# Kernel optimization log

Measured on AMD Instinct MI355X. Metric: run time of the kernel, lower is better.

Reference implementation:

```python
import jax, jax.numpy as jnp
import numpy as np

BINS = 32
NUM_ACTION = 12


def _conv(x, w, b, stride, pad):
    y = jax.lax.conv_general_dilated(x, w, (stride, stride), [(pad, pad), (pad, pad)],
                                     dimension_numbers=('NCHW', 'OIHW', 'NCHW'))
    return y + b[None, :, None, None]


def _maxpool3s2(x):
    return jax.lax.reduce_window(x, -jnp.inf, jax.lax.max, (1, 1, 3, 3), (1, 1, 2, 2), 'VALID')


def _area_resize(x, oh, ow):
    b, c, h, w = x.shape  # exact area interp when h%oh==0, w%ow==0
    return x.reshape(b, c, oh, h // oh, ow, w // ow).mean(axis=(3, 5))


def _sobel_mag(gray):
    # kornia.filters.Sobel: normalized sobel kernels (abs-sum=1), replicate pad, sqrt(gx^2+gy^2+eps)
    kx = jnp.array([[-1., 0., 1.], [-2., 0., 2.], [-1., 0., 1.]], jnp.float32) / 8.0
    k = jnp.stack([kx, kx.T])[:, None]  # [2,1,3,3]
    p = jnp.pad(gray, ((0, 0), (0, 0), (1, 1), (1, 1)), mode='edge')
    g = jax.lax.conv_general_dilated(p, k, (1, 1), 'VALID',
                                     dimension_numbers=('NCHW', 'OIHW', 'NCHW'))
    return jnp.sqrt(jnp.sum(g * g, axis=1, keepdims=True) + 1e-6)


def _hist_feature(img):
    # Fused replacement for FeatureExtractor's python triple-loop of torch.histc calls.
    # img: [B,1,H,W] with values in [0,1]. Scale 0: whole-image hist; scale 1: the 4
    # quadrants of the full-res image; third bins-slot stays zero (loop only runs 2 scales).
    b, _, h, w = img.shape
    idx = jnp.clip((img[:, 0] * BINS).astype(jnp.int32), 0, BINS - 1)  # [B,H,W]
    hist = lambda i: jnp.zeros((BINS,), jnp.float32).at[i.ravel()].add(1.0)
    h0 = jax.vmap(hist)(idx) / (h * w)                                  # [B,BINS]
    h2, w2 = h // 2, w // 2
    blocks = idx.reshape(b, 2, h2, 2, w2).transpose(0, 1, 3, 2, 4).reshape(b * 4, h2 * w2)
    h1 = jax.vmap(hist)(blocks).reshape(b, 2, 2, BINS) / (h2 * w2)      # [B,2,2,BINS]
    out0 = jnp.broadcast_to(h0[:, :, None, None], (b, BINS, 4, 4))
    out1 = jnp.repeat(jnp.repeat(h1.transpose(0, 3, 1, 2), 2, axis=2), 2, axis=3)
    out2 = jnp.zeros_like(out0)
    return jnp.concatenate([out0, out1, out2], axis=1)                  # [B,3*BINS,4,4]


def _l2norm(x):
    return x / (jnp.linalg.norm(x, axis=1, keepdims=True) + 1e-7)


def _forward(image, w1, b1, w2, b2, w3, b3, w4, b4, w5, b5, fc1_w, fc1_b, fc2_w, fc2_b):
    b = image.shape[0]
    rgb = jnp.stack([image[:, 0], 0.5 * (image[:, 1] + image[:, 2]), image[:, 3]], axis=1)
    # AlexNet conv backbone on area-resized 112x112 -> [B,256,2,2]
    x = _area_resize(rgb, 112, 112)
    x = _maxpool3s2(jax.nn.relu(_conv(x, w1, b1, 4, 2)))
    x = _maxpool3s2(jax.nn.relu(_conv(x, w2, b2, 1, 2)))
    x = jax.nn.relu(_conv(x, w3, b3, 1, 1))
    x = jax.nn.relu(_conv(x, w4, b4, 1, 1))
    x = _maxpool3s2(jax.nn.relu(_conv(x, w5, b5, 1, 1)))
    f_sem = x.reshape(b, -1)                                            # [B,1024]
    gray = (0.299 * rgb[:, 0] + 0.587 * rgb[:, 1] + 0.114 * rgb[:, 2])[:, None]
    f_inten = _hist_feature(gray).reshape(b, -1)                        # [B,1536]
    f_grad = _hist_feature(_sobel_mag(gray)).reshape(b, -1)             # [B,1536]
    f_cat = jnp.concatenate([_l2norm(f_sem), _l2norm(f_inten), _l2norm(f_grad)], axis=1)
    h = jax.nn.relu(f_cat)                                              # Dropout = identity (eval)
    h = jax.nn.relu(h @ fc1_w.T + fc1_b)
    return h @ fc2_w.T + fc2_b                                          # [B,NUM_ACTION]


def setup_inputs() -> dict:
    key = jax.random.key(0)
    ks = jax.random.split(key, 8)
    B = 64
    image = jax.random.uniform(ks[0], (B, 4, 448, 448), jnp.float32)
    w = lambda k, shape, s=0.02: jax.random.normal(k, shape, jnp.float32) * s
    return {
        'image': image,
        'w1': w(ks[1], (64, 3, 11, 11)), 'b1': jnp.zeros((64,), jnp.float32),
        'w2': w(ks[2], (192, 64, 5, 5)), 'b2': jnp.zeros((192,), jnp.float32),
        'w3': w(ks[3], (384, 192, 3, 3)), 'b3': jnp.zeros((384,), jnp.float32),
        'w4': w(ks[4], (256, 384, 3, 3)), 'b4': jnp.zeros((256,), jnp.float32),
        'w5': w(ks[5], (256, 256, 3, 3)), 'b5': jnp.zeros((256,), jnp.float32),
        'fc1_w': w(ks[6], (256, 4096), 0.01), 'fc1_b': jnp.zeros((256,), jnp.float32),
        'fc2_w': w(ks[7], (NUM_ACTION, 256), 0.05), 'fc2_b': jnp.zeros((NUM_ACTION,), jnp.float32),
    }


def reference(image, w1, b1, w2, b2, w3, b3, w4, b4, w5, b5, fc1_w, fc1_b, fc2_w, fc2_b):
    return _forward(image, w1, b1, w2, b2, w3, b3, w4, b4, w5, b5, fc1_w, fc1_b, fc2_w, fc2_b)
```

## Files before the change

kernel.cpp:

```cpp
#include <hip/hip_runtime.h>
#include <math.h>

typedef __attribute__((ext_vector_type(8))) short short8;
typedef __attribute__((ext_vector_type(8))) unsigned short u16x8;
typedef __attribute__((ext_vector_type(4))) float f32x4;
typedef unsigned short ushort_t;

constexpr size_t OFF_HINT = 0;
constexpr size_t OFF_HGRD = OFF_HINT + (size_t)64*160;
constexpr size_t OFF_F    = OFF_HGRD + (size_t)64*160;
constexpr size_t OFF_H1   = OFF_F    + (size_t)64*4096;
constexpr size_t OFF_P5   = OFF_H1   + (size_t)64*256;
constexpr size_t OFF_WHI  = OFF_P5   + (size_t)64*1024;
constexpr size_t W1_OFF = 0;         constexpr int K1T = 363,  K1R = 384;
constexpr size_t W2_OFF = 24576;     constexpr int K2T = 1600, K2R = 1664;
constexpr size_t W3_OFF = 344064;    constexpr int K3T = 1728, K3R = 1792;
constexpr size_t W4_OFF = 1032192;   constexpr int K4T = 3456, K4R = 3456;
constexpr size_t W5_OFF = 1916928;   constexpr int K5T = 2304, K5R = 2304;
constexpr size_t WP_U16 = 2506752;
constexpr size_t OFF_WLO  = OFF_WHI + WP_U16/2;
constexpr size_t OFF_RA   = OFF_WLO + WP_U16/2;
constexpr size_t SZ_RA    = (size_t)2583552/2;
constexpr size_t A4P_U16  = 786432;
constexpr size_t OFF_RB   = OFF_RA + SZ_RA;
constexpr size_t SZ_RB    = (size_t)2985984/2;
constexpr size_t WS_FLOATS = OFF_RB + SZ_RB;

__device__ __forceinline__ void bf16split(float v, unsigned short& hi, unsigned short& lo) {
  union { float f; unsigned u; } a; a.f = v;
  unsigned uh = (a.u + 0x7FFFu + ((a.u >> 16) & 1u)) >> 16;
  hi = (unsigned short)uh;
  union { unsigned u; float f; } b; b.u = uh << 16;
  float rem = v - b.f;
  union { float f; unsigned u; } c; c.f = rem;
  lo = (unsigned short)((c.u + 0x7FFFu + ((c.u >> 16) & 1u)) >> 16);
}
__device__ __forceinline__ ushort_t f2bf(float f) {
  union { float f; unsigned u; } a; a.f = f;
  return (ushort_t)((a.u + 0x7FFFu + ((a.u >> 16) & 1u)) >> 16);
}
__device__ __forceinline__ float bf2f(ushort_t u) {
  union { unsigned u; float f; } a; a.u = ((unsigned)u) << 16; return a.f;
}

__global__ __launch_bounds__(256) void k_wsplit_all(const float* __restrict__ w1,
                                                    const float* __restrict__ w2,
                                                    const float* __restrict__ w3,
                                                    const float* __restrict__ w4,
                                                    const float* __restrict__ w5,
                                                    ushort_t* __restrict__ whi,
                                                    ushort_t* __restrict__ wlo) {
  const size_t idx = (size_t)blockIdx.x * 256 + threadIdx.x;
  if (idx >= WP_U16) return;
  const float* w; int kt, kr; size_t base;
  if (idx < W2_OFF)                { w = w1; kt = K1T; kr = K1R; base = W1_OFF; }
  else if (idx < W3_OFF)           { w = w2; kt = K2T; kr = K2R; base = W2_OFF; }
  else if (idx < W4_OFF)           { w = w3; kt = K3T; kr = K3R; base = W3_OFF; }
  else if (idx < W5_OFF)           { w = w4; kt = K4T; kr = K4R; base = W4_OFF; }
  else                             { w = w5; kt = K5T; kr = K5R; base = W5_OFF; }
  const size_t rel = idx - base;
  const int m = (int)(rel / kr), k = (int)(rel - (size_t)m * kr);
  const float v = (k < kt) ? w[(size_t)m * kt + k] : 0.f;
  unsigned short h, l;
  bf16split(v, h, l);
  whi[idx] = h; wlo[idx] = l;
}

__global__ __launch_bounds__(256) void k_preproc(const float* __restrict__ img,
                                                 float* __restrict__ hint,
                                                 float* __restrict__ hgrd,
                                                 ushort_t* __restrict__ x0) {
  const int b = blockIdx.x, s = blockIdx.y;
  const int r0 = s * 8;
  __shared__ float gs[10][448];
  __shared__ unsigned char lh[128 * 260];
  __shared__ float part[8 * 112 * 3];
  const int tid = threadIdx.x;
  for (int i = tid; i < (128 * 260) / 4; i += 256) ((unsigned*)lh)[i] = 0u;
  const float* ib = img + (size_t)b * 4 * 200704;
  for (int i = tid; i < 10 * 112; i += 256) {
    const int rr = i / 112, cc = i % 112, c4 = cc * 4;
    int r = r0 + rr - 1; r = r < 0 ? 0 : (r > 447 ? 447 : r);
    const size_t o = (size_t)r * 448 + c4;
    const float4 vr = *(const float4*)&ib[o];
    const float4 g1 = *(const float4*)&ib[200704 + o];
    const float4 g2 = *(const float4*)&ib[2 * 200704 + o];
    const float4 vb = *(const float4*)&ib[3 * 200704 + o];
    float4 g;
    g.x = 0.299f * vr.x + 0.587f * (0.5f * (g1.x + g2.x)) + 0.114f * vb.x;
    g.y = 0.299f * vr.y + 0.587f * (0.5f * (g1.y + g2.y)) + 0.114f * vb.y;
    g.z = 0.299f * vr.z + 0.587f * (0.5f * (g1.z + g2.z)) + 0.114f * vb.z;
    g.w = 0.299f * vr.w + 0.587f * (0.5f * (g1.w + g2.w)) + 0.114f * vb.w;
    *(float4*)&gs[rr][c4] = g;
    if (rr >= 1 && rr <= 8) {
      const float sr = vr.x + vr.y + vr.z + vr.w;
      const float sg = 0.5f * (g1.x + g2.x) + 0.5f * (g1.y + g2.y)
                     + 0.5f * (g1.z + g2.z) + 0.5f * (g1.w + g2.w);
      const float sb = vb.x + vb.y + vb.z + vb.w;
      float* pp = &part[((rr - 1) * 112 + cc) * 3];
      pp[0] = sr; pp[1] = sg; pp[2] = sb;
    }
  }
  __syncthreads();
  for (int i = tid; i < 8 * 112; i += 256) {
    const int dr = i / 112, c4 = (i % 112) * 4;
    const unsigned colbit = (c4 >= 224) ? 1u : 0u;
    const int cl = c4 > 0 ? c4 - 1 : 0;
    const int cr = c4 < 444 ? c4 + 4 : 447;
    const float4 m0 = *(const float4*)&gs[dr][c4];
    const float4 m1 = *(const float4*)&gs[dr + 1][c4];
    const float4 m2 = *(const float4*)&gs[dr + 2][c4];
    const float r0v[6] = {gs[dr][cl],     m0.x, m0.y, m0.z, m0.w, gs[dr][cr]};
    const float r1v[6] = {gs[dr + 1][cl], m1.x, m1.y, m1.z, m1.w, gs[dr + 1][cr]};
    const float r2v[6] = {gs[dr + 2][cl], m2.x, m2.y, m2.z, m2.w, gs[dr + 2][cr]};
    #pragma unroll
    for (int j = 0; j < 4; ++j) {
      const float g = r1v[j + 1];
      int bin = (int)(g * 32.f); bin = bin > 31 ? 31 : (bin < 0 ? 0 : bin);
      lh[(colbit * 32u + (unsigned)bin) * 260u + (unsigned)tid]++;
      const float gx = (-r0v[j] + r0v[j + 2] - 2.f * r1v[j] + 2.f * r1v[j + 2]
                        - r2v[j] + r2v[j + 2]) * 0.125f;
      const float gy = (-r0v[j] - 2.f * r0v[j + 1] - r0v[j + 2]
                        + r2v[j] + 2.f * r2v[j + 1] + r2v[j + 2]) * 0.125f;
      const float mag = sqrtf(gx * gx + gy * gy + 1e-6f);
      int sb = (int)(mag * 32.f); sb = sb > 31 ? 31 : (sb < 0 ? 0 : sb);
      lh[(64u + colbit * 32u + (unsigned)sb) * 260u + (unsigned)tid]++;
    }
  }
  __syncthreads();
  {
    const unsigned rowbit = (s >= 28) ? 1u : 0u;
    const int key = tid >> 1, half = tid & 1;
    const unsigned* row = (const unsigned*)&lh[(unsigned)key * 260u];
    unsigned sum = 0;
    #pragma unroll
    for (int d = 0; d < 32; ++d) {
      const unsigned v = row[half * 32 + d];
      sum += (v & 0xFFu) + ((v >> 8) & 0xFFu) + ((v >> 16) & 0xFFu) + (v >> 24);
    }
    sum += __shfl_down(sum, 1, 64);
    if (half == 0) {
      const int type = key >> 6;
      const int rest = key & 63;
      const int colbit2 = rest >> 5, bin = rest & 31;
      float* dst = (type ? hgrd : hint) + (size_t)b * 160 + 32 + (rowbit * 2 + colbit2) * 32 + bin;
      atomicAdd(dst, (float)sum);
    }
  }
  for (int i = tid; i < 672; i += 256) {
    const int cc = i % 112;
    const int t  = i / 112;
    const int or2 = t & 1, ch = t >> 1;
    float sum = 0.f;
    #pragma unroll
    for (int rw = 0; rw < 4; ++rw)
      sum += part[((or2 * 4 + rw) * 112 + cc) * 3 + ch];
    x0[(((size_t)b * 3 + ch) * 116 + 2 + 2 * s + or2) * 116 + 2 + cc] = f2bf(sum * (1.f / 16.f));
  }
}

template<int CIN, int HP, int WP, int KH, int KW, int STRIDE, int OH, int OW,
         int OHP, int OWP, int OPAD, int M, int MT>
__global__ __launch_bounds__(512) void k_conv_mfma(const ushort_t* __restrict__ in,
                                                   const ushort_t* __restrict__ whi_,
                                                   const ushort_t* __restrict__ wlo_,
                                                   const float* __restrict__ bias,
                                                   ushort_t* __restrict__ out) {
  constexpr int K_TOT  = CIN * KH * KW;
  constexpr int K_ROUND = ((K_TOT + 127) / 128) * 128;
  constexpr int GSTEPS = K_ROUND / 128;
  constexpr int KHW = KH * KW;
  constexpr int NPB = OH * OW;
  constexpr int WROWS = MT / 16;
  constexpr int TGRP  = 4 / WROWS;
  constexpr int TFRAG = 4 / TGRP;
  __shared__ ushort_t Bs[2][64 * 64];
  __shared__ ushort_t ftab[K_ROUND];
  const int tid = threadIdx.x;
  const int lane = tid & 63, wv = tid >> 6;
  const int g = wv >> 2, wg = wv & 3;
  const int sub = tid & 255;
  const int n0 = blockIdx.x * 64, m0 = blockIdx.y * MT;
  for (int k = tid; k < K_ROUND; k += 512) {
    const int c = k / KHW, kr = k - c * KHW;
    const int ky = kr / KW, kx = kr - (kr / KW) * KW;
    ftab[k] = (k < K_TOT) ? (ushort_t)(2 * ((c * HP + ky) * WP + kx)) : (ushort_t)0;
  }
  const int col = sub & 63, kc2 = sub >> 6;
  const int nb = n0 + col;
  const int bB = nb / NPB, rB = nb % NPB;
  const int oyB = rB / OW, oxB = rB % OW;
  const char* baseB = (const char*)(in + (size_t)bB * CIN * HP * WP)
                      + 2 * (oyB * STRIDE * WP + oxB * STRIDE);
  const int wm = wg % WROWS, tg = wg / WROWS;
  const int mrow = m0 + wm * 16 + (lane & 15);
  const ushort_t* wh = whi_ + (size_t)mrow * K_ROUND;
  const ushort_t* wl = wlo_ + (size_t)mrow * K_ROUND;
  const int kA = (lane >> 4) * 8;
  f32x4 acc[TFRAG] = {};
  __syncthreads();
  const int kb0 = g * GSTEPS * 64;
  for (int step = 0; step < GSTEPS; ++step) {
    const int kb = kb0 + step * 64;
    const u16x8 f0 = *(const u16x8*)&ftab[kb + kc2 * 16];
    const u16x8 f1 = *(const u16x8*)&ftab[kb + kc2 * 16 + 8];
    u16x8 b0, b1;
    #pragma unroll
    for (int j = 0; j < 8; ++j) b0[j] = *(const ushort_t*)(baseB + f0[j]);
    #pragma unroll
    for (int j = 0; j < 8; ++j) b1[j] = *(const ushort_t*)(baseB + f1[j]);
    const int c0 = kc2 * 2, c1 = c0 + 1;
    *(u16x8*)&Bs[g][col * 64 + ((c0 ^ (col & 7)) * 8)] = b0;
    *(u16x8*)&Bs[g][col * 64 + ((c1 ^ (col & 7)) * 8)] = b1;
    __syncthreads();
    #pragma unroll
    for (int s = 0; s < 2; ++s) {
      const int kk = kb + s * 32 + kA;
      const short8 a_h = *(const short8*)&wh[kk];
      const short8 a_l = *(const short8*)&wl[kk];
      const int cA = s * 4 + (lane >> 4);
      #pragma unroll
      for (int tt = 0; tt < TFRAG; ++tt) {
        const int t = tg * TFRAG + tt;
        const int coln = t * 16 + (lane & 15);
        const short8 b_v = *(const short8*)&Bs[g][coln * 64 + ((cA ^ (coln & 7)) * 8)];
        acc[tt] = __builtin_amdgcn_mfma_f32_16x16x32_bf16(a_h, b_v, acc[tt], 0, 0, 0);
        acc[tt] = __builtin_amdgcn_mfma_f32_16x16x32_bf16(a_l, b_v, acc[tt], 0, 0, 0);
      }
    }
    __syncthreads();
  }
  float* scratch = (float*)&Bs[0][0];
  if (g == 1) {
    #pragma unroll
    for (int tt = 0; tt < TFRAG; ++tt) {
      const int t = tg * TFRAG + tt;
      #pragma unroll
      for (int q = 0; q < 4; ++q)
        scratch[(wm * 16 + (lane >> 4) * 4 + q) * 64 + t * 16 + (lane & 15)] = acc[tt][q];
    }
  }
  __syncthreads();
  if (g == 0) {
    #pragma unroll
    for (int q = 0; q < 4; ++q) {
      const int m = m0 + wm * 16 + (lane >> 4) * 4 + q;
      const float bi = bias[m];
      #pragma unroll
      for (int tt = 0; tt < TFRAG; ++tt) {
        const int t = tg * TFRAG + tt;
        const int n = n0 + t * 16 + (lane & 15);
        const float v = acc[tt][q]
                      + scratch[(wm * 16 + (lane >> 4) * 4 + q) * 64 + t * 16 + (lane & 15)]
                      + bi;
        const int b = n / NPB, r = n % NPB;
        const int oy = r / OW, ox = r - (r / OW) * OW;
        out[(((size_t)b * M + m) * OHP + OPAD + oy) * OWP + OPAD + ox] = f2bf(fmaxf(v, 0.f));
      }
    }
  }
}

template<int C, int HI, int HO, int HOP, int PAD, bool OUTF32>
__global__ __launch_bounds__(256) void k_pool(const ushort_t* __restrict__ in,
                                              void* __restrict__ out) {
  const int idx = blockIdx.x * 256 + threadIdx.x;
  constexpr int TOT = 64 * C * HOP * HOP;
  if (idx >= TOT) return;
  const int x = idx % HOP;
  const int y = (idx / HOP) % HOP;
  const int c = (idx / (HOP * HOP)) % C;
  const int b = idx / (HOP * HOP * C);
  ushort_t v = 0;
  const int oy = y - PAD, ox = x - PAD;
  if (oy >= 0 && oy < HO && ox >= 0 && ox < HO) {
    const ushort_t* ib = in + (size_t)(b * C + c) * HI * HI + (size_t)(oy * 2) * HI + ox * 2;
    #pragma unroll
    for (int i = 0; i < 3; ++i)
      #pragma unroll
      for (int j = 0; j < 3; ++j) {
        const ushort_t u = ib[i * HI + j];
        v = u > v ? u : v;
      }
  }
  if constexpr (OUTF32) ((float*)out)[idx] = bf2f(v);
  else                  ((ushort_t*)out)[idx] = v;
}

__global__ __launch_bounds__(256) void k_feat(const float* __restrict__ p5,
                                              const float* __restrict__ hint,
                                              const float* __restrict__ hgrad,
                                              float* __restrict__ f) {
  const int b = blockIdx.x, tid = threadIdx.x;
  __shared__ float tmp4[4];
  __shared__ float vals[160];
  const float* ps = p5 + (size_t)b * 1024;
  float* fb = f + (size_t)b * 4096;
  float mv[4]; float ss = 0.f;
  #pragma unroll
  for (int i = 0; i < 4; ++i) { mv[i] = ps[tid + i * 256]; ss += mv[i] * mv[i]; }
  #pragma unroll
  for (int o = 32; o > 0; o >>= 1) ss += __shfl_down(ss, o, 64);
  if ((tid & 63) == 0) tmp4[tid >> 6] = ss;
  __syncthreads();
  const float inv = 1.f / (sqrtf(tmp4[0] + tmp4[1] + tmp4[2] + tmp4[3]) + 1e-7f);
  #pragma unroll
  for (int i = 0; i < 4; ++i) fb[tid + i * 256] = fmaxf(mv[i] * inv, 0.f);
  for (int ft = 0; ft < 2; ++ft) {
    const float* hb = (ft ? hgrad : hint) + (size_t)b * 160;
    __syncthreads();
    if (tid < 160) {
      float cnt;
      if (tid < 32) cnt = hb[32 + tid] + hb[64 + tid] + hb[96 + tid] + hb[128 + tid];
      else          cnt = hb[tid];
      vals[tid] = cnt * (tid < 32 ? (1.f / 200704.f) : (1.f / 50176.f));
    }
    __syncthreads();
    float s2 = 0.f;
    if (tid < 160) s2 = (tid < 32 ? 16.f : 4.f) * vals[tid] * vals[tid];
    #pragma unroll
    for (int o = 32; o > 0; o >>= 1) s2 += __shfl_down(s2, o, 64);
    __syncthreads();
    if ((tid & 63) == 0) tmp4[tid >> 6] = s2;
    __syncthreads();
    const float inv2 = 1.f / (sqrtf(tmp4[0] + tmp4[1] + tmp4[2] + tmp4[3]) + 1e-7f);
    float* fo = fb + 1024 + ft * 1536;
    for (int idx = tid; idx < 1536; idx += 256) {
      const int ch = idx >> 4, i2 = (idx >> 2) & 3, j = idx & 3;
      float v;
      if (ch < 32)      v = vals[ch];
      else if (ch < 64) v = vals[32 + (((i2 >> 1) * 2) + (j >> 1)) * 32 + (ch - 32)];
      else              v = 0.f;
      fo[idx] = fmaxf(v * inv2, 0.f);
    }
  }
}

__global__ __launch_bounds__(256) void k_fc1(const float* __restrict__ f,
                                             const float* __restrict__ w,
                                             const float* __restrict__ bias,
                                             float* __restrict__ h1) {
  const int gid = blockIdx.x * 4 + (threadIdx.x >> 6);
  const int lane = threadIdx.x & 63;
  if (gid >= 64 * 256) return;
  const int oc = gid & 255, b = gid >> 8;
  const float* fb = f + (size_t)b * 4096;
  const float* wr = w + (size_t)oc * 4096;
  float s = 0.f;
  for (int k = lane; k < 4096; k += 64) s += fb[k] * wr[k];
  #pragma unroll
  for (int o = 32; o > 0; o >>= 1) s += __shfl_down(s, o, 64);
  if (lane == 0) h1[(size_t)b * 256 + oc] = fmaxf(s + bias[oc], 0.f);
}

__global__ __launch_bounds__(256) void k_fc2_simple(const float* __restrict__ h1,
                                                    const float* __restrict__ w,
                                                    const float* __restrict__ bias,
                                                    float* __restrict__ out) {
  const int idx = blockIdx.x * 256 + threadIdx.x;
  if (idx >= 64 * 12) return;
  const int oc = idx % 12, b = idx / 12;
  const float* hb = h1 + (size_t)b * 256;
  const float* wr = w + (size_t)oc * 256;
  float s = bias[oc];
  for (int k = 0; k < 256; ++k) s += hb[k] * wr[k];
  out[b * 12 + oc] = s;
}

extern "C" void kernel_launch(void* const* d_in, const int* in_sizes, int n_in,
                              void* d_out, int out_size, void* d_ws, size_t ws_size,
                              hipStream_t stream) {
  const float* img  = (const float*)d_in[0];
  const float* w1 = (const float*)d_in[1];  const float* b1 = (const float*)d_in[2];
  const float* w2 = (const float*)d_in[3];  const float* b2 = (const float*)d_in[4];
  const float* w3 = (const float*)d_in[5];  const float* b3 = (const float*)d_in[6];
  const float* w4 = (const float*)d_in[7];  const float* b4 = (const float*)d_in[8];
  const float* w5 = (const float*)d_in[9];  const float* b5 = (const float*)d_in[10];
  const float* fc1w = (const float*)d_in[11]; const float* fc1b = (const float*)d_in[12];
  const float* fc2w = (const float*)d_in[13]; const float* fc2b = (const float*)d_in[14];
  float* out = (float*)d_out;
  float* ws  = (float*)d_ws;

  float* hint = ws + OFF_HINT;
  float* hgrd = ws + OFF_HGRD;
  float* f    = ws + OFF_F;
  float* h1   = ws + OFF_H1;
  float* p5   = ws + OFF_P5;
  ushort_t* whi = (ushort_t*)(ws + OFF_WHI);
  ushort_t* wlo = (ushort_t*)(ws + OFF_WLO);
  ushort_t* ra  = (ushort_t*)(ws + OFF_RA);
  ushort_t* rb  = (ushort_t*)(ws + OFF_RB);

  hipMemsetAsync(hint, 0, (size_t)2 * 64 * 160 * sizeof(float), stream);
  hipMemsetAsync(ra, 0, (size_t)64 * 3 * 116 * 116 * 2, stream);

  k_wsplit_all<<<(int)((WP_U16 + 255) / 256), 256, 0, stream>>>(w1, w2, w3, w4, w5, whi, wlo);

  k_preproc<<<dim3(64, 56), 256, 0, stream>>>(img, hint, hgrd, ra);

  k_conv_mfma<3,116,116,11,11,4,27,27,27,27,0,64,64>
      <<<dim3(729, 1), 512, 0, stream>>>(ra, whi + W1_OFF, wlo + W1_OFF, b1, rb);
  k_pool<64,27,13,17,2,false><<<(64*64*17*17 + 255)/256, 256, 0, stream>>>(rb, ra);
  k_conv_mfma<64,17,17,5,5,1,13,13,13,13,0,192,64>
      <<<dim3(169, 3), 512, 0, stream>>>(ra, whi + W2_OFF, wlo + W2_OFF, b2, rb);
  k_pool<192,13,6,8,1,false><<<(64*192*8*8 + 255)/256, 256, 0, stream>>>(rb, ra);
  hipMemsetAsync(rb, 0, (size_t)64*384*8*8*2, stream);
  hipMemsetAsync(ra + A4P_U16, 0, (size_t)64*256*8*8*2, stream);
  k_conv_mfma<192,8,8,3,3,1,6,6,8,8,1,384,32>
      <<<dim3(36, 12), 512, 0, stream>>>(ra, whi + W3_OFF, wlo + W3_OFF, b3, rb);
  k_conv_mfma<384,8,8,3,3,1,6,6,8,8,1,256,32>
      <<<dim3(36, 8), 512, 0, stream>>>(rb, whi + W4_OFF, wlo + W4_OFF, b4, ra + A4P_U16);
  k_conv_mfma<256,8,8,3,3,1,6,6,6,6,0,256,32>
      <<<dim3(36, 8), 512, 0, stream>>>(ra + A4P_U16, whi + W5_OFF, wlo + W5_OFF, b5, rb);
  k_pool<256,6,2,2,0,true><<<(64*256*2*2 + 255)/256, 256, 0, stream>>>(rb, p5);

  k_feat<<<64, 256, 0, stream>>>(p5, hint, hgrd, f);
  k_fc1<<<(64*256)/4, 256, 0, stream>>>(f, fc1w, fc1b, h1);
  k_fc2_simple<<<(64*12 + 255)/256, 256, 0, stream>>>(h1, fc2w, fc2b, out);
}
```

Baseline: 445.5 us.

## Double-buffer conv im2col tiles with register prefetch and halve preproc LDS

The MFMA conv kernel now keeps two LDS buffers per K-group and prefetches the next step's gathered B values and A weight fragments into registers while the MFMAs for the current step run. This replaces two barriers per step with one and hides global-load latency. The preprocessing kernel splits the intensity and gradient histograms into two passes over a halved byte-counter buffer, and stores the pooled partial sums as bf16, to cut LDS use and raise occupancy. The costs are a doubled conv LDS footprint, more registers, an extra histogram pass, and a small precision loss in the pooled input sums.

```diff
diff --git a/kernel.cpp b/kernel.cpp
--- a/kernel.cpp
+++ b/kernel.cpp
@@ -73,10 +73,10 @@
   const int b = blockIdx.x, s = blockIdx.y;
   const int r0 = s * 8;
   __shared__ float gs[10][448];
-  __shared__ unsigned char lh[128 * 260];
-  __shared__ float part[8 * 112 * 3];
+  __shared__ unsigned char lh[64 * 260];
+  __shared__ ushort_t part[8 * 112 * 3];
   const int tid = threadIdx.x;
-  for (int i = tid; i < (128 * 260) / 4; i += 256) ((unsigned*)lh)[i] = 0u;
+  for (int i = tid; i < (64 * 260) / 4; i += 256) ((unsigned*)lh)[i] = 0u;
   const float* ib = img + (size_t)b * 4 * 200704;
   for (int i = tid; i < 10 * 112; i += 256) {
     const int rr = i / 112, cc = i % 112, c4 = cc * 4;
@@ -97,10 +97,52 @@
       const float sg = 0.5f * (g1.x + g2.x) + 0.5f * (g1.y + g2.y)
                      + 0.5f * (g1.z + g2.z) + 0.5f * (g1.w + g2.w);
       const float sb = vb.x + vb.y + vb.z + vb.w;
-      float* pp = &part[((rr - 1) * 112 + cc) * 3];
-      pp[0] = sr; pp[1] = sg; pp[2] = sb;
-    }
-  }
+      ushort_t* pp = &part[((rr - 1) * 112 + cc) * 3];
+      pp[0] = f2bf(sr); pp[1] = f2bf(sg); pp[2] = f2bf(sb);
+    }
+  }
+  __syncthreads();
+  for (int i = tid; i < 672; i += 256) {
+    const int cc = i % 112;
+    const int t  = i / 112;
+    const int or2 = t & 1, ch = t >> 1;
+    float sum = 0.f;
+    #pragma unroll
+    for (int rw = 0; rw < 4; ++rw)
+      sum += bf2f(part[((or2 * 4 + rw) * 112 + cc) * 3 + ch]);
+    x0[(((size_t)b * 3 + ch) * 116 + 2 + 2 * s + or2) * 116 + 2 + cc] = f2bf(sum * (1.f / 16.f));
+  }
+  for (int i = tid; i < 8 * 112; i += 256) {
+    const int dr = i / 112, c4 = (i % 112) * 4;
+    const unsigned colbit = (c4 >= 224) ? 1u : 0u;
+    const float4 m1 = *(const float4*)&gs[dr + 1][c4];
+    const float gv[4] = {m1.x, m1.y, m1.z, m1.w};
+    #pragma unroll
+    for (int j = 0; j < 4; ++j) {
+      int bin = (int)(gv[j] * 32.f); bin = bin > 31 ? 31 : (bin < 0 ? 0 : bin);
+      lh[(colbit * 32u + (unsigned)bin) * 260u + (unsigned)tid]++;
+    }
+  }
+  __syncthreads();
+  const unsigned rowbit = (s >= 28) ? 1u : 0u;
+  {
+    const int key = tid >> 2, quarter = tid & 3;
+    const unsigned* row = (const unsigned*)&lh[(unsigned)key * 260u];
+    unsigned sum = 0;
+    #pragma unroll
+    for (int d = 0; d < 16; ++d) {
+      const unsigned v = row[quarter * 16 + d];
+      sum += (v & 0xFFu) + ((v >> 8) & 0xFFu) + ((v >> 16) & 0xFFu) + (v >> 24);
+    }
+    sum += __shfl_down(sum, 1, 64);
+    sum += __shfl_down(sum, 2, 64);
+    if (quarter == 0) {
+      const int colbit2 = key >> 5, bin = key & 31;
+      atomicAdd(&hint[(size_t)b * 160 + 32 + (rowbit * 2 + colbit2) * 32 + bin], (float)sum);
+    }
+  }
+  __syncthreads();
+  for (int i = tid; i < (64 * 260) / 4; i += 256) ((unsigned*)lh)[i] = 0u;
   __syncthreads();
   for (int i = tid; i < 8 * 112; i += 256) {
     const int dr = i / 112, c4 = (i % 112) * 4;
@@ -115,47 +157,31 @@
     const float r2v[6] = {gs[dr + 2][cl], m2.x, m2.y, m2.z, m2.w, gs[dr + 2][cr]};
     #pragma unroll
     for (int j = 0; j < 4; ++j) {
-      const float g = r1v[j + 1];
-      int bin = (int)(g * 32.f); bin = bin > 31 ? 31 : (bin < 0 ? 0 : bin);
-      lh[(colbit * 32u + (unsigned)bin) * 260u + (unsigned)tid]++;
       const float gx = (-r0v[j] + r0v[j + 2] - 2.f * r1v[j] + 2.f * r1v[j + 2]
                         - r2v[j] + r2v[j + 2]) * 0.125f;
       const float gy = (-r0v[j] - 2.f * r0v[j + 1] - r0v[j + 2]
                         + r2v[j] + 2.f * r2v[j + 1] + r2v[j + 2]) * 0.125f;
       const float mag = sqrtf(gx * gx + gy * gy + 1e-6f);
       int sb = (int)(mag * 32.f); sb = sb > 31 ? 31 : (sb < 0 ? 0 : sb);
-      lh[(64u + colbit * 32u + (unsigned)sb) * 260u + (unsigned)tid]++;
+      lh[(colbit * 32u + (unsigned)sb) * 260u + (unsigned)tid]++;
     }
   }
   __syncthreads();
   {
-    const unsigned rowbit = (s >= 28) ? 1u : 0u;
-    const int key = tid >> 1, half = tid & 1;
+    const int key = tid >> 2, quarter = tid & 3;
     const unsigned* row = (const unsigned*)&lh[(unsigned)key * 260u];
     unsigned sum = 0;
     #pragma unroll
-    for (int d = 0; d < 32; ++d) {
-      const unsigned v = row[half * 32 + d];
+    for (int d = 0; d < 16; ++d) {
+      const unsigned v = row[quarter * 16 + d];
       sum += (v & 0xFFu) + ((v >> 8) & 0xFFu) + ((v >> 16) & 0xFFu) + (v >> 24);
     }
     sum += __shfl_down(sum, 1, 64);
-    if (half == 0) {
-      const int type = key >> 6;
-      const int rest = key & 63;
-      const int colbit2 = rest >> 5, bin = rest & 31;
-      float* dst = (type ? hgrd : hint) + (size_t)b * 160 + 32 + (rowbit * 2 + colbit2) * 32 + bin;
-      atomicAdd(dst, (float)sum);
-    }
-  }
-  for (int i = tid; i < 672; i += 256) {
-    const int cc = i % 112;
-    const int t  = i / 112;
-    const int or2 = t & 1, ch = t >> 1;
-    float sum = 0.f;
-    #pragma unroll
-    for (int rw = 0; rw < 4; ++rw)
-      sum += part[((or2 * 4 + rw) * 112 + cc) * 3 + ch];
-    x0[(((size_t)b * 3 + ch) * 116 + 2 + 2 * s + or2) * 116 + 2 + cc] = f2bf(sum * (1.f / 16.f));
+    sum += __shfl_down(sum, 2, 64);
+    if (quarter == 0) {
+      const int colbit2 = key >> 5, bin = key & 31;
+      atomicAdd(&hgrd[(size_t)b * 160 + 32 + (rowbit * 2 + colbit2) * 32 + bin], (float)sum);
+    }
   }
 }
 
@@ -174,7 +200,7 @@
   constexpr int WROWS = MT / 16;
   constexpr int TGRP  = 4 / WROWS;
   constexpr int TFRAG = 4 / TGRP;
-  __shared__ ushort_t Bs[2][64 * 64];
+  __shared__ ushort_t Bs[2][2][64 * 64];
   __shared__ ushort_t ftab[K_ROUND];
   const int tid = threadIdx.x;
   const int lane = tid & 63, wv = tid >> 6;
@@ -198,39 +224,70 @@
   const ushort_t* wl = wlo_ + (size_t)mrow * K_ROUND;
   const int kA = (lane >> 4) * 8;
   f32x4 acc[TFRAG] = {};
-  __syncthreads();
   const int kb0 = g * GSTEPS * 64;
-  for (int step = 0; step < GSTEPS; ++step) {
-    const int kb = kb0 + step * 64;
+  __syncthreads();
+
+  u16x8 rb0, rb1;
+  short8 rah0, ral0, rah1, ral1;
+  {
+    const int kb = kb0;
     const u16x8 f0 = *(const u16x8*)&ftab[kb + kc2 * 16];
     const u16x8 f1 = *(const u16x8*)&ftab[kb + kc2 * 16 + 8];
-    u16x8 b0, b1;
-    #pragma unroll
-    for (int j = 0; j < 8; ++j) b0[j] = *(const ushort_t*)(baseB + f0[j]);
-    #pragma unroll
-    for (int j = 0; j < 8; ++j) b1[j] = *(const ushort_t*)(baseB + f1[j]);
+    #pragma unroll
+    for (int j = 0; j < 8; ++j) rb0[j] = *(const ushort_t*)(baseB + f0[j]);
+    #pragma unroll
+    for (int j = 0; j < 8; ++j) rb1[j] = *(const ushort_t*)(baseB + f1[j]);
+    rah0 = *(const short8*)&wh[kb + kA];
+    ral0 = *(const short8*)&wl[kb + kA];
+    rah1 = *(const short8*)&wh[kb + 32 + kA];
+    ral1 = *(const short8*)&wl[kb + 32 + kA];
+  }
+  {
     const int c0 = kc2 * 2, c1 = c0 + 1;
-    *(u16x8*)&Bs[g][col * 64 + ((c0 ^ (col & 7)) * 8)] = b0;
-    *(u16x8*)&Bs[g][col * 64 + ((c1 ^ (col & 7)) * 8)] = b1;
-    __syncthreads();
+    *(u16x8*)&Bs[g][0][col * 64 + ((c0 ^ (col & 7)) * 8)] = rb0;
+    *(u16x8*)&Bs[g][0][col * 64 + ((c1 ^ (col & 7)) * 8)] = rb1;
+  }
+  __syncthreads();
+  int cur = 0;
+  for (int step = 0; step < GSTEPS; ++step) {
+    const short8 a_h0 = rah0, a_l0 = ral0, a_h1 = rah1, a_l1 = ral1;
+    if (step + 1 < GSTEPS) {
+      const int kb = kb0 + (step + 1) * 64;
+      const u16x8 f0 = *(const u16x8*)&ftab[kb + kc2 * 16];
+      const u16x8 f1 = *(const u16x8*)&ftab[kb + kc2 * 16 + 8];
+      #pragma unroll
+      for (int j = 0; j < 8; ++j) rb0[j] = *(const ushort_t*)(baseB + f0[j]);
+      #pragma unroll
+      for (int j = 0; j < 8; ++j) rb1[j] = *(const ushort_t*)(baseB + f1[j]);
+      rah0 = *(const short8*)&wh[kb + kA];
+      ral0 = *(const short8*)&wl[kb + kA];
+      rah1 = *(const short8*)&wh[kb + 32 + kA];
+      ral1 = *(const short8*)&wl[kb + 32 + kA];
+    }
     #pragma unroll
     for (int s = 0; s < 2; ++s) {
-      const int kk = kb + s * 32 + kA;
-      const short8 a_h = *(const short8*)&wh[kk];
-      const short8 a_l = *(const short8*)&wl[kk];
+      const short8 a_h = s ? a_h1 : a_h0;
+      const short8 a_l = s ? a_l1 : a_l0;
       const int cA = s * 4 + (lane >> 4);
       #pragma unroll
       for (int tt = 0; tt < TFRAG; ++tt) {
         const int t = tg * TFRAG + tt;
         const int coln = t * 16 + (lane & 15);
-        const short8 b_v = *(const short8*)&Bs[g][coln * 64 + ((cA ^ (coln & 7)) * 8)];
+        const short8 b_v = *(const short8*)&Bs[g][cur][coln * 64 + ((cA ^ (coln & 7)) * 8)];
         acc[tt] = __builtin_amdgcn_mfma_f32_16x16x32_bf16(a_h, b_v, acc[tt], 0, 0, 0);
         acc[tt] = __builtin_amdgcn_mfma_f32_16x16x32_bf16(a_l, b_v, acc[tt], 0, 0, 0);
       }
     }
-    __syncthreads();
-  }
-  float* scratch = (float*)&Bs[0][0];
+    if (step + 1 < GSTEPS) {
+      const int c0 = kc2 * 2, c1 = c0 + 1;
+      *(u16x8*)&Bs[g][cur ^ 1][col * 64 + ((c0 ^ (col & 7)) * 8)] = rb0;
+      *(u16x8*)&Bs[g][cur ^ 1][col * 64 + ((c1 ^ (col & 7)) * 8)] = rb1;
+      __syncthreads();
+      cur ^= 1;
+    }
+  }
+  __syncthreads();
+  float* scratch = (float*)&Bs[0][0][0];
   if (g == 1) {
     #pragma unroll
     for (int tt = 0; tt < TFRAG; ++tt) {
```

Result: no change. 446.7 us (+0.3%).
